# Performance work log

Hardware: AMD Instinct MI355X
Metric: run time of the kernel (lower is better)

Reference implementation:

```python
import jax, jax.numpy as jnp
import numpy as np

N_NODES = 100000


def gcn_conv(x, W, b, src, dst, num_nodes):
    """PyG GCNConv: add self-loops, symmetric deg^{-1/2} normalization,
    linear transform, scatter-add aggregation (source -> target), bias."""
    h = x @ W  # [N, out]
    # degree on target nodes, counting the added self-loop (+1)
    deg = jax.ops.segment_sum(jnp.ones_like(dst, dtype=h.dtype), dst,
                              num_segments=num_nodes) + 1.0
    dinv = jax.lax.rsqrt(deg)  # deg >= 1 always
    norm = dinv[src] * dinv[dst]  # [E]
    agg = jax.ops.segment_sum(h[src] * norm[:, None], dst,
                              num_segments=num_nodes)
    # self-loop contribution: norm_ii = dinv[i]^2
    out = agg + h * (dinv * dinv)[:, None]
    return out + b


def setup_inputs() -> dict:
    key = jax.random.key(0)
    ks = jax.random.split(key, 8)
    num_features, hidden, emb = 64, 64, 32
    x = jax.random.normal(ks[0], (N_NODES, num_features), dtype=jnp.float32)
    edge_index = jax.random.randint(ks[1], (2, 1600000), 0, N_NODES, dtype=jnp.int64)
    def glorot(k, shape):
        lim = float(np.sqrt(6.0 / (shape[0] + shape[1])))
        return jax.random.uniform(k, shape, jnp.float32, -lim, lim)
    return {
        "x": x,
        "edge_index": edge_index,
        "W1": glorot(ks[2], (num_features, hidden)),
        "b1": jnp.zeros((hidden,), jnp.float32),
        "W2": glorot(ks[3], (hidden, hidden)),
        "b2": jnp.zeros((hidden,), jnp.float32),
        "Wf": glorot(ks[4], (hidden, emb)),
        "bf": jnp.zeros((emb,), jnp.float32),
    }


def reference(x, edge_index, W1, b1, W2, b2, Wf, bf):
    src, dst = edge_index[0], edge_index[1]
    n = x.shape[0]
    h = gcn_conv(x, W1, b1, src, dst, n)
    h = jax.nn.relu(h)  # dropout is identity in eval mode
    h = gcn_conv(h, W2, b2, src, dst, n)
    h = jax.nn.relu(h)
    return h @ Wf + bf
```

## Files before the change

kernel.cpp:

```cpp
#include <hip/hip_runtime.h>


#define NODE_SHIFT 9
#define NODES_PER_BKT 512
#define K1PAD 208
#define NB_PART 256
#define HPAD 68

__device__ __forceinline__ unsigned short f2bf_rne(float f) {
    unsigned int u = __float_as_uint(f);
    unsigned int r = (u + 0x7FFFu + ((u >> 16) & 1u)) >> 16;
    return (unsigned short)r;
}
__device__ __forceinline__ float bf_lo(unsigned int u) {
    return __uint_as_float(u << 16);
}
__device__ __forceinline__ float bf_hi(unsigned int u) {
    return __uint_as_float(u & 0xFFFF0000u);
}

__global__ __launch_bounds__(256) void coarse_hist_kernel(const int* __restrict__ dst, int E,
                                                          int* __restrict__ bkt_partial,
                                                          int K1, int CHK) {
    __shared__ int lcnt[256];
    const int tid = threadIdx.x;
    const int start = blockIdx.x * CHK;
    const int end = min(E, start + CHK);
    for (int k = tid; k < 256; k += 256) lcnt[k] = 0;
    __syncthreads();
    const int s4 = start >> 2;
    const int e4 = end >> 2;
    for (int i = s4 + tid; i < e4; i += 256) {
        const int4 d = ((const int4*)dst)[i];
        atomicAdd(&lcnt[d.x >> NODE_SHIFT], 1);
        atomicAdd(&lcnt[d.y >> NODE_SHIFT], 1);
        atomicAdd(&lcnt[d.z >> NODE_SHIFT], 1);
        atomicAdd(&lcnt[d.w >> NODE_SHIFT], 1);
    }
    __syncthreads();
    for (int k = tid; k < K1; k += 256)
        bkt_partial[blockIdx.x * K1PAD + k] = lcnt[k];
}

__global__ __launch_bounds__(256) void bucket_scan_kernel(const int* __restrict__ bkt_partial,
                                                          int* __restrict__ bkt_start,
                                                          int* __restrict__ bkt_cursor,
                                                          int K1, int E) {
    __shared__ int wsum[4];
    const int tid = threadIdx.x;
    const int lane = tid & 63;
    const int wave = tid >> 6;
    int c = 0;
    if (tid < K1)
        for (int b = 0; b < NB_PART; b++) c += bkt_partial[b * K1PAD + tid];
    int inc = c;
#pragma unroll
    for (int o = 1; o < 64; o <<= 1) {
        int t = __shfl_up(inc, o, 64);
        if (lane >= o) inc += t;
    }
    if (lane == 63) wsum[wave] = inc;
    __syncthreads();
    int wpre = 0;
#pragma unroll
    for (int w = 0; w < 4; w++) wpre += (w < wave) ? wsum[w] : 0;
    const int p = wpre + inc - c;
    if (tid < K1) { bkt_start[tid] = p; bkt_cursor[tid] = p; }
    if (tid == 0) bkt_start[K1] = E;
}

__global__ __launch_bounds__(256) void partition_kernel(const int* __restrict__ src,
                                                        const int* __restrict__ dst, int E,
                                                        int* __restrict__ bkt_cursor,
                                                        int2* __restrict__ staging,
                                                        int K1, int CHK) {
    __shared__ int lcnt[256];
    __shared__ int lcur[256];
    const int tid = threadIdx.x;
    const int start = blockIdx.x * CHK;
    const int end = min(E, start + CHK);
    for (int k = tid; k < 256; k += 256) lcnt[k] = 0;
    __syncthreads();
    const int s4 = start >> 2;
    const int e4 = end >> 2;
    for (int i = s4 + tid; i < e4; i += 256) {
        const int4 d = ((const int4*)dst)[i];
        atomicAdd(&lcnt[d.x >> NODE_SHIFT], 1);
        atomicAdd(&lcnt[d.y >> NODE_SHIFT], 1);
        atomicAdd(&lcnt[d.z >> NODE_SHIFT], 1);
        atomicAdd(&lcnt[d.w >> NODE_SHIFT], 1);
    }
    __syncthreads();
    for (int k = tid; k < K1; k += 256) {
        int cc = lcnt[k];
        lcur[k] = cc ? atomicAdd(&bkt_cursor[k], cc) : 0;
    }
    __syncthreads();
    for (int i = s4 + tid; i < e4; i += 256) {
        const int4 d = ((const int4*)dst)[i];
        const int4 s = ((const int4*)src)[i];
        int pos;
        pos = atomicAdd(&lcur[d.x >> NODE_SHIFT], 1); staging[pos] = make_int2(d.x, s.x);
        pos = atomicAdd(&lcur[d.y >> NODE_SHIFT], 1); staging[pos] = make_int2(d.y, s.y);
        pos = atomicAdd(&lcur[d.z >> NODE_SHIFT], 1); staging[pos] = make_int2(d.z, s.z);
        pos = atomicAdd(&lcur[d.w >> NODE_SHIFT], 1); staging[pos] = make_int2(d.w, s.w);
    }
}

__global__ __launch_bounds__(512) void bucket_build_kernel(const int2* __restrict__ staging,
                                                           const int* __restrict__ bkt_start,
                                                           float* __restrict__ dinv,
                                                           int* __restrict__ offs,
                                                           int* __restrict__ csr_src,
                                                           int N, int E) {
    __shared__ int cnt[NODES_PER_BKT];
    __shared__ int wsum[8];
    const int tid = threadIdx.x;
    const int node0 = blockIdx.x * NODES_PER_BKT;
    const int estart = bkt_start[blockIdx.x];
    const int eend = bkt_start[blockIdx.x + 1];

    cnt[tid] = 0;
    __syncthreads();
    for (int e = estart + tid; e < eend; e += 512)
        atomicAdd(&cnt[staging[e].x - node0], 1);
    __syncthreads();

    const int lane = tid & 63;
    const int wave = tid >> 6;
    const int c = cnt[tid];
    int inc = c;
#pragma unroll
    for (int o = 1; o < 64; o <<= 1) {
        int t = __shfl_up(inc, o, 64);
        if (lane >= o) inc += t;
    }
    if (lane == 63) wsum[wave] = inc;
    __syncthreads();
    int wpre = 0;
#pragma unroll
    for (int w = 0; w < 8; w++) wpre += (w < wave) ? wsum[w] : 0;
    const int p = estart + wpre + inc - c;

    const int node = node0 + tid;
    __syncthreads();
    if (node < N) {
        offs[node] = p;
        dinv[node] = rsqrtf((float)c + 1.0f);
    }
    cnt[tid] = p;
    __syncthreads();
    for (int e = estart + tid; e < eend; e += 512) {
        int2 r = staging[e];
        int pos = atomicAdd(&cnt[r.x - node0], 1);
        csr_src[pos] = r.y;
    }
    if (blockIdx.x == 0 && tid == 0) offs[N] = E;
}

__global__ __launch_bounds__(256) void gemm1_kernel(const float* __restrict__ X,
                                                    const float* __restrict__ W,
                                                    const float* __restrict__ dinv,
                                                    unsigned short* __restrict__ Y, int N) {
    constexpr int OUTC = 64, RPT = 8;
    constexpr int R = 128;
    constexpr int RPAD = R + (R / 32) * 4;
    __shared__ float Ws[64 * OUTC];
    __shared__ float Xt[64 * RPAD];

    const int tid = threadIdx.x;
    const int row0 = blockIdx.x * R;

    for (int l = tid; l < 64 * OUTC / 4; l += 256)
        ((float4*)Ws)[l] = ((const float4*)W)[l];

    for (int l = tid; l < R * 16; l += 256) {
        const int r = l & (R - 1);
        const int kq = l >> 7;
        float4 v = make_float4(0.f, 0.f, 0.f, 0.f);
        const int row = row0 + r;
        if (row < N) v = ((const float4*)(X + (long)row * 64))[kq];
        const int rp = r + (r >> 5) * 4;
        Xt[(4 * kq + 0) * RPAD + rp] = v.x;
        Xt[(4 * kq + 1) * RPAD + rp] = v.y;
        Xt[(4 * kq + 2) * RPAD + rp] = v.z;
        Xt[(4 * kq + 3) * RPAD + rp] = v.w;
    }
    __syncthreads();

    const int cg = tid % 16;
    const int rg = tid / 16;
    const int c0 = cg * 4;
    const int r0 = rg * RPT;
    const int r0p = r0 + (r0 >> 5) * 4;

    float acc[RPT][4];
#pragma unroll
    for (int i = 0; i < RPT; i++)
#pragma unroll
        for (int j = 0; j < 4; j++) acc[i][j] = 0.f;

#pragma unroll 4
    for (int k = 0; k < 64; k++) {
        float xv[RPT];
        const float4 xa = *(const float4*)&Xt[k * RPAD + r0p];
        const float4 xb = *(const float4*)&Xt[k * RPAD + r0p + 4];
        xv[0] = xa.x; xv[1] = xa.y; xv[2] = xa.z; xv[3] = xa.w;
        xv[4] = xb.x; xv[5] = xb.y; xv[6] = xb.z; xv[7] = xb.w;
        const float4 wa = *(const float4*)&Ws[k * OUTC + c0];
        const float wv[4] = {wa.x, wa.y, wa.z, wa.w};
#pragma unroll
        for (int i = 0; i < RPT; i++)
#pragma unroll
            for (int j = 0; j < 4; j++)
                acc[i][j] += xv[i] * wv[j];
    }

#pragma unroll
    for (int i = 0; i < RPT; i++) {
        const int row = row0 + r0 + i;
        if (row < N) {
            const float sc = dinv[row];
            ushort4 o16;
            o16.x = f2bf_rne(acc[i][0] * sc);
            o16.y = f2bf_rne(acc[i][1] * sc);
            o16.z = f2bf_rne(acc[i][2] * sc);
            o16.w = f2bf_rne(acc[i][3] * sc);
            *(ushort4*)&Y[(long)row * OUTC + c0] = o16;
        }
    }
}

template <int OUTC, bool HEAD>
__global__ __launch_bounds__(256) void fused_agg_gemm_kernel(
    const unsigned short* __restrict__ T, const int* __restrict__ offs,
    const int* __restrict__ csr_src, const float* __restrict__ dinv,
    const float* __restrict__ aggbias, const float* __restrict__ W,
    const float* __restrict__ headbias, void* __restrict__ Yv, int N) {
    __shared__ float Ws[64 * OUTC];
    __shared__ float hs[32 * HPAD];

    const int tid = threadIdx.x;

    for (int l = tid; l < 64 * OUTC / 4; l += 256)
        ((float4*)Ws)[l] = ((const float4*)W)[l];

    const int nl = tid >> 3;
    const int node = blockIdx.x * 32 + nl;
    const int l8 = tid & 7;
    const int fo = l8 * 8;

    float o[8];
    if (node < N) {
        const int start = offs[node];
        const int n_edges = offs[node + 1] - start;
        const int* ep = csr_src + start;

        float acc[8];
#pragma unroll
        for (int j = 0; j < 8; j++) acc[j] = 0.f;

#define ACC_U4(v)                                       \
    do {                                                \
        acc[0] += bf_lo((v).x); acc[1] += bf_hi((v).x); \
        acc[2] += bf_lo((v).y); acc[3] += bf_hi((v).y); \
        acc[4] += bf_lo((v).z); acc[5] += bf_hi((v).z); \
        acc[6] += bf_lo((v).w); acc[7] += bf_hi((v).w); \
    } while (0)

        int s[8];
        int e = 0;
        if (n_edges >= 8) {
#pragma unroll
            for (int j = 0; j < 8; j++) s[j] = ep[j];
            while (true) {
                uint4 h[8];
#pragma unroll
                for (int j = 0; j < 8; j++)
                    h[j] = *(const uint4*)&T[(long)s[j] * 64 + fo];
                const int next = e + 8;
                const bool more = (next + 8 <= n_edges);
                if (more) {
#pragma unroll
                    for (int j = 0; j < 8; j++) s[j] = ep[next + j];
                }
#pragma unroll
                for (int j = 0; j < 8; j++) ACC_U4(h[j]);
                e = next;
                if (!more) break;
            }
        }
        if (e + 4 <= n_edges) {
            int s4[4];
#pragma unroll
            for (int j = 0; j < 4; j++) s4[j] = ep[e + j];
            uint4 h[4];
#pragma unroll
            for (int j = 0; j < 4; j++)
                h[j] = *(const uint4*)&T[(long)s4[j] * 64 + fo];
#pragma unroll
            for (int j = 0; j < 4; j++) ACC_U4(h[j]);
            e += 4;
        }
        for (; e < n_edges; e++) {
            const uint4 hv = *(const uint4*)&T[(long)ep[e] * 64 + fo];
            ACC_U4(hv);
        }
#undef ACC_U4

        const float di = dinv[node];
        const uint4 sv = *(const uint4*)&T[(long)node * 64 + fo];
        const float self[8] = {bf_lo(sv.x), bf_hi(sv.x), bf_lo(sv.y), bf_hi(sv.y),
                               bf_lo(sv.z), bf_hi(sv.z), bf_lo(sv.w), bf_hi(sv.w)};
        const float4 ba = *(const float4*)&aggbias[fo];
        const float4 bb = *(const float4*)&aggbias[fo + 4];
        const float bv[8] = {ba.x, ba.y, ba.z, ba.w, bb.x, bb.y, bb.z, bb.w};
#pragma unroll
        for (int j = 0; j < 8; j++)
            o[j] = fmaxf(di * (acc[j] + self[j]) + bv[j], 0.f);
    } else {
#pragma unroll
        for (int j = 0; j < 8; j++) o[j] = 0.f;
    }
    float* hp = &hs[nl * HPAD + fo];
    *(float4*)hp = make_float4(o[0], o[1], o[2], o[3]);
    *(float4*)(hp + 4) = make_float4(o[4], o[5], o[6], o[7]);
    __syncthreads();

    constexpr int CPT = OUTC / 8;
    const int row = blockIdx.x * 32 + (tid >> 3);
    const int c0 = (tid & 7) * CPT;
    const int lrow = tid >> 3;

    float acc2[CPT];
#pragma unroll
    for (int j = 0; j < CPT; j++) acc2[j] = 0.f;

#pragma unroll 4
    for (int k = 0; k < 64; k++) {
        const float x = hs[lrow * HPAD + k];
        const float4 wa = *(const float4*)&Ws[k * OUTC + c0];
        acc2[0] += x * wa.x;
        acc2[1] += x * wa.y;
        acc2[2] += x * wa.z;
        acc2[3] += x * wa.w;
        if (CPT == 8) {
            const float4 wb = *(const float4*)&Ws[k * OUTC + c0 + 4];
            acc2[4] += x * wb.x;
            acc2[5] += x * wb.y;
            acc2[6] += x * wb.z;
            acc2[7] += x * wb.w;
        }
    }

    if (row < N) {
        if (HEAD) {
            const float4 hb = *(const float4*)&headbias[c0];
            float* yp = &((float*)Yv)[(long)row * OUTC + c0];
            *(float4*)yp = make_float4(acc2[0] + hb.x, acc2[1] + hb.y,
                                       acc2[2] + hb.z, acc2[3] + hb.w);
        } else {
            const float sc = dinv[row];
            unsigned short* yp = &((unsigned short*)Yv)[(long)row * OUTC + c0];
            ushort4 o0, o1;
            o0.x = f2bf_rne(acc2[0] * sc); o0.y = f2bf_rne(acc2[1] * sc);
            o0.z = f2bf_rne(acc2[2] * sc); o0.w = f2bf_rne(acc2[3] * sc);
            o1.x = f2bf_rne(acc2[4] * sc); o1.y = f2bf_rne(acc2[5] * sc);
            o1.z = f2bf_rne(acc2[6] * sc); o1.w = f2bf_rne(acc2[7] * sc);
            *(ushort4*)yp = o0;
            *(ushort4*)(yp + 4) = o1;
        }
    }
}

extern "C" void kernel_launch(void* const* d_in, const int* in_sizes, int n_in,
                              void* d_out, int out_size, void* d_ws, size_t ws_size,
                              hipStream_t stream) {
    const float* x  = (const float*)d_in[0];
    const int*   ei = (const int*)d_in[1];
    const float* W1 = (const float*)d_in[2];
    const float* b1 = (const float*)d_in[3];
    const float* W2 = (const float*)d_in[4];
    const float* b2 = (const float*)d_in[5];
    const float* Wf = (const float*)d_in[6];
    const float* bf = (const float*)d_in[7];

    const int N = in_sizes[0] / 64;
    const int E = in_sizes[1] / 2;
    const int* src = ei;
    const int* dst = ei + E;
    const int K1 = (N + NODES_PER_BKT - 1) / NODES_PER_BKT;

    char* ws = (char*)d_ws;
    size_t off = 0;
    auto alloc = [&](size_t bytes) -> void* {
        void* p = ws + off;
        off = (off + bytes + 255) & ~(size_t)255;
        return p;
    };
    int*   bkt_partial = (int*)alloc((size_t)NB_PART * K1PAD * 4);
    int*   bkt_start   = (int*)alloc(257 * 4);
    int*   bkt_cursor  = (int*)alloc(256 * 4);
    float* dinv        = (float*)alloc((size_t)N * 4);
    int*   offs        = (int*)alloc((size_t)(N + 1) * 4);
    int*   csr_src     = (int*)alloc((size_t)E * 4);
    unsigned short* A  = (unsigned short*)alloc((size_t)N * 64 * 2);
    unsigned short* A2 = (unsigned short*)alloc((size_t)N * 64 * 2);
    int2*  staging     = (int2*)alloc((size_t)E * 8);

    const int NB = NB_PART;
    const int CHK = ((E / 4 + NB - 1) / NB) * 4;

    coarse_hist_kernel<<<NB, 256, 0, stream>>>(dst, E, bkt_partial, K1, CHK);
    bucket_scan_kernel<<<1, 256, 0, stream>>>(bkt_partial, bkt_start, bkt_cursor, K1, E);
    partition_kernel<<<NB, 256, 0, stream>>>(src, dst, E, bkt_cursor, staging, K1, CHK);
    bucket_build_kernel<<<K1, 512, 0, stream>>>(staging, bkt_start, dinv, offs, csr_src, N, E);

    gemm1_kernel<<<(N + 127) / 128, 256, 0, stream>>>(x, W1, dinv, A, N);

    fused_agg_gemm_kernel<64, false><<<(N + 31) / 32, 256, 0, stream>>>(
        A, offs, csr_src, dinv, b1, W2, nullptr, A2, N);

    fused_agg_gemm_kernel<32, true><<<(N + 31) / 32, 256, 0, stream>>>(
        A2, offs, csr_src, dinv, b2, Wf, bf, d_out, N);
}
```

Measured before the change: 230.1 us.

## Use fixed-capacity buckets and packed 32-bit staging to drop histogram and scan passes

Result: slower. 260.6 us (+13.3%).

```diff
diff --git a/kernel.cpp b/kernel.cpp
--- a/kernel.cpp
+++ b/kernel.cpp
@@ -3,7 +3,7 @@
 
 #define NODE_SHIFT 9
 #define NODES_PER_BKT 512
-#define K1PAD 208
+#define BKT_CAP 9216
 #define NB_PART 256
 #define HPAD 68
 
@@ -19,10 +19,13 @@
     return __uint_as_float(u & 0xFFFF0000u);
 }
 
-__global__ __launch_bounds__(256) void coarse_hist_kernel(const int* __restrict__ dst, int E,
-                                                          int* __restrict__ bkt_partial,
-                                                          int K1, int CHK) {
+__global__ __launch_bounds__(256) void partition_kernel(const int* __restrict__ src,
+                                                        const int* __restrict__ dst, int E,
+                                                        int* __restrict__ bkt_cursor,
+                                                        unsigned int* __restrict__ staging,
+                                                        int K1, int CHK) {
     __shared__ int lcnt[256];
+    __shared__ int lcur[256];
     const int tid = threadIdx.x;
     const int start = blockIdx.x * CHK;
     const int end = min(E, start + CHK);
@@ -38,92 +41,45 @@
         atomicAdd(&lcnt[d.w >> NODE_SHIFT], 1);
     }
     __syncthreads();
-    for (int k = tid; k < K1; k += 256)
-        bkt_partial[blockIdx.x * K1PAD + k] = lcnt[k];
-}
-
-__global__ __launch_bounds__(256) void bucket_scan_kernel(const int* __restrict__ bkt_partial,
-                                                          int* __restrict__ bkt_start,
-                                                          int* __restrict__ bkt_cursor,
-                                                          int K1, int E) {
-    __shared__ int wsum[4];
-    const int tid = threadIdx.x;
-    const int lane = tid & 63;
-    const int wave = tid >> 6;
-    int c = 0;
-    if (tid < K1)
-        for (int b = 0; b < NB_PART; b++) c += bkt_partial[b * K1PAD + tid];
-    int inc = c;
-#pragma unroll
-    for (int o = 1; o < 64; o <<= 1) {
-        int t = __shfl_up(inc, o, 64);
-        if (lane >= o) inc += t;
-    }
-    if (lane == 63) wsum[wave] = inc;
-    __syncthreads();
-    int wpre = 0;
-#pragma unroll
-    for (int w = 0; w < 4; w++) wpre += (w < wave) ? wsum[w] : 0;
-    const int p = wpre + inc - c;
-    if (tid < K1) { bkt_start[tid] = p; bkt_cursor[tid] = p; }
-    if (tid == 0) bkt_start[K1] = E;
-}
-
-__global__ __launch_bounds__(256) void partition_kernel(const int* __restrict__ src,
-                                                        const int* __restrict__ dst, int E,
-                                                        int* __restrict__ bkt_cursor,
-                                                        int2* __restrict__ staging,
-                                                        int K1, int CHK) {
-    __shared__ int lcnt[256];
-    __shared__ int lcur[256];
-    const int tid = threadIdx.x;
-    const int start = blockIdx.x * CHK;
-    const int end = min(E, start + CHK);
-    for (int k = tid; k < 256; k += 256) lcnt[k] = 0;
-    __syncthreads();
-    const int s4 = start >> 2;
-    const int e4 = end >> 2;
-    for (int i = s4 + tid; i < e4; i += 256) {
-        const int4 d = ((const int4*)dst)[i];
-        atomicAdd(&lcnt[d.x >> NODE_SHIFT], 1);
-        atomicAdd(&lcnt[d.y >> NODE_SHIFT], 1);
-        atomicAdd(&lcnt[d.z >> NODE_SHIFT], 1);
-        atomicAdd(&lcnt[d.w >> NODE_SHIFT], 1);
-    }
-    __syncthreads();
     for (int k = tid; k < K1; k += 256) {
-        int cc = lcnt[k];
-        lcur[k] = cc ? atomicAdd(&bkt_cursor[k], cc) : 0;
+        int c = lcnt[k];
+        int g = c ? atomicAdd(&bkt_cursor[k], c) : 0;
+        lcur[k] = k * BKT_CAP + g;
     }
     __syncthreads();
     for (int i = s4 + tid; i < e4; i += 256) {
         const int4 d = ((const int4*)dst)[i];
         const int4 s = ((const int4*)src)[i];
         int pos;
-        pos = atomicAdd(&lcur[d.x >> NODE_SHIFT], 1); staging[pos] = make_int2(d.x, s.x);
-        pos = atomicAdd(&lcur[d.y >> NODE_SHIFT], 1); staging[pos] = make_int2(d.y, s.y);
-        pos = atomicAdd(&lcur[d.z >> NODE_SHIFT], 1); staging[pos] = make_int2(d.z, s.z);
-        pos = atomicAdd(&lcur[d.w >> NODE_SHIFT], 1); staging[pos] = make_int2(d.w, s.w);
-    }
-}
-
-__global__ __launch_bounds__(512) void bucket_build_kernel(const int2* __restrict__ staging,
-                                                           const int* __restrict__ bkt_start,
+        pos = atomicAdd(&lcur[d.x >> NODE_SHIFT], 1);
+        staging[pos] = ((unsigned int)(d.x & (NODES_PER_BKT - 1)) << 17) | (unsigned int)s.x;
+        pos = atomicAdd(&lcur[d.y >> NODE_SHIFT], 1);
+        staging[pos] = ((unsigned int)(d.y & (NODES_PER_BKT - 1)) << 17) | (unsigned int)s.y;
+        pos = atomicAdd(&lcur[d.z >> NODE_SHIFT], 1);
+        staging[pos] = ((unsigned int)(d.z & (NODES_PER_BKT - 1)) << 17) | (unsigned int)s.z;
+        pos = atomicAdd(&lcur[d.w >> NODE_SHIFT], 1);
+        staging[pos] = ((unsigned int)(d.w & (NODES_PER_BKT - 1)) << 17) | (unsigned int)s.w;
+    }
+}
+
+__global__ __launch_bounds__(512) void bucket_build_kernel(const unsigned int* __restrict__ staging,
+                                                           const int* __restrict__ bkt_cursor,
                                                            float* __restrict__ dinv,
                                                            int* __restrict__ offs,
+                                                           int* __restrict__ n_e,
                                                            int* __restrict__ csr_src,
-                                                           int N, int E) {
+                                                           int N) {
     __shared__ int cnt[NODES_PER_BKT];
     __shared__ int wsum[8];
     const int tid = threadIdx.x;
     const int node0 = blockIdx.x * NODES_PER_BKT;
-    const int estart = bkt_start[blockIdx.x];
-    const int eend = bkt_start[blockIdx.x + 1];
+    const int estart = blockIdx.x * BKT_CAP;
+    const int eend = estart + bkt_cursor[blockIdx.x];
 
     cnt[tid] = 0;
     __syncthreads();
     for (int e = estart + tid; e < eend; e += 512)
-        atomicAdd(&cnt[staging[e].x - node0], 1);
+        atomicAdd(&cnt[staging[e] >> 17], 1);
     __syncthreads();
 
     const int lane = tid & 63;
@@ -146,16 +102,16 @@
     __syncthreads();
     if (node < N) {
         offs[node] = p;
+        n_e[node] = c;
         dinv[node] = rsqrtf((float)c + 1.0f);
     }
     cnt[tid] = p;
     __syncthreads();
     for (int e = estart + tid; e < eend; e += 512) {
-        int2 r = staging[e];
-        int pos = atomicAdd(&cnt[r.x - node0], 1);
-        csr_src[pos] = r.y;
-    }
-    if (blockIdx.x == 0 && tid == 0) offs[N] = E;
+        const unsigned int r = staging[e];
+        int pos = atomicAdd(&cnt[r >> 17], 1);
+        csr_src[pos] = (int)(r & 0x1FFFFu);
+    }
 }
 
 __global__ __launch_bounds__(256) void gemm1_kernel(const float* __restrict__ X,
@@ -234,16 +190,13 @@
 template <int OUTC, bool HEAD>
 __global__ __launch_bounds__(256) void fused_agg_gemm_kernel(
     const unsigned short* __restrict__ T, const int* __restrict__ offs,
-    const int* __restrict__ csr_src, const float* __restrict__ dinv,
-    const float* __restrict__ aggbias, const float* __restrict__ W,
-    const float* __restrict__ headbias, void* __restrict__ Yv, int N) {
-    __shared__ float Ws[64 * OUTC];
+    const int* __restrict__ n_e, const int* __restrict__ csr_src,
+    const float* __restrict__ dinv, const float* __restrict__ aggbias,
+    const float* __restrict__ W, const float* __restrict__ headbias,
+    void* __restrict__ Yv, int N) {
     __shared__ float hs[32 * HPAD];
 
     const int tid = threadIdx.x;
-
-    for (int l = tid; l < 64 * OUTC / 4; l += 256)
-        ((float4*)Ws)[l] = ((const float4*)W)[l];
 
     const int nl = tid >> 3;
     const int node = blockIdx.x * 32 + nl;
@@ -253,7 +206,7 @@
     float o[8];
     if (node < N) {
         const int start = offs[node];
-        const int n_edges = offs[node + 1] - start;
+        const int n_edges = n_e[node];
         const int* ep = csr_src + start;
 
         float acc[8];
@@ -339,13 +292,13 @@
 #pragma unroll 4
     for (int k = 0; k < 64; k++) {
         const float x = hs[lrow * HPAD + k];
-        const float4 wa = *(const float4*)&Ws[k * OUTC + c0];
+        const float4 wa = *(const float4*)&W[k * OUTC + c0];
         acc2[0] += x * wa.x;
         acc2[1] += x * wa.y;
         acc2[2] += x * wa.z;
         acc2[3] += x * wa.w;
         if (CPT == 8) {
-            const float4 wb = *(const float4*)&Ws[k * OUTC + c0 + 4];
+            const float4 wb = *(const float4*)&W[k * OUTC + c0 + 4];
             acc2[4] += x * wb.x;
             acc2[5] += x * wb.y;
             acc2[6] += x * wb.z;
@@ -398,29 +351,27 @@
         off = (off + bytes + 255) & ~(size_t)255;
         return p;
     };
-    int*   bkt_partial = (int*)alloc((size_t)NB_PART * K1PAD * 4);
-    int*   bkt_start   = (int*)alloc(257 * 4);
     int*   bkt_cursor  = (int*)alloc(256 * 4);
     float* dinv        = (float*)alloc((size_t)N * 4);
-    int*   offs        = (int*)alloc((size_t)(N + 1) * 4);
-    int*   csr_src     = (int*)alloc((size_t)E * 4);
+    int*   offs        = (int*)alloc((size_t)N * 4);
+    int*   n_e         = (int*)alloc((size_t)N * 4);
+    unsigned int* staging = (unsigned int*)alloc((size_t)K1 * BKT_CAP * 4);
+    int*   csr_src     = (int*)alloc((size_t)K1 * BKT_CAP * 4);
     unsigned short* A  = (unsigned short*)alloc((size_t)N * 64 * 2);
     unsigned short* A2 = (unsigned short*)alloc((size_t)N * 64 * 2);
-    int2*  staging     = (int2*)alloc((size_t)E * 8);
 
     const int NB = NB_PART;
     const int CHK = ((E / 4 + NB - 1) / NB) * 4;
 
-    coarse_hist_kernel<<<NB, 256, 0, stream>>>(dst, E, bkt_partial, K1, CHK);
-    bucket_scan_kernel<<<1, 256, 0, stream>>>(bkt_partial, bkt_start, bkt_cursor, K1, E);
+    hipMemsetAsync(bkt_cursor, 0, (size_t)K1 * 4, stream);
     partition_kernel<<<NB, 256, 0, stream>>>(src, dst, E, bkt_cursor, staging, K1, CHK);
-    bucket_build_kernel<<<K1, 512, 0, stream>>>(staging, bkt_start, dinv, offs, csr_src, N, E);
+    bucket_build_kernel<<<K1, 512, 0, stream>>>(staging, bkt_cursor, dinv, offs, n_e, csr_src, N);
 
     gemm1_kernel<<<(N + 127) / 128, 256, 0, stream>>>(x, W1, dinv, A, N);
 
     fused_agg_gemm_kernel<64, false><<<(N + 31) / 32, 256, 0, stream>>>(
-        A, offs, csr_src, dinv, b1, W2, nullptr, A2, N);
+        A, offs, n_e, csr_src, dinv, b1, W2, nullptr, A2, N);
 
     fused_agg_gemm_kernel<32, true><<<(N + 31) / 32, 256, 0, stream>>>(
-        A2, offs, csr_src, dinv, b2, Wf, bf, d_out, N);
-}
+        A2, offs, n_e, csr_src, dinv, b2, Wf, bf, d_out, N);
+}
```
